# Kernel optimization log

Measured on AMD Instinct MI355X. Metric: run time of the kernel, lower is better.

Reference implementation:

```python
import jax, jax.numpy as jnp
import numpy as np

N = 100000        # num_nodes
F_IN = 512        # node_features
F_OUT = 2         # GCNConv out channels (hardcoded in module)
E = 3200000       # num edges (avg degree 32)


def setup_inputs() -> dict:
    key = jax.random.key(0)
    k = jax.random.split(key, 8)
    x = jax.random.normal(k[0], (N, F_IN), dtype=jnp.float32)
    edge_list = jax.random.randint(k[1], (2, E), 0, N, dtype=jnp.int64)
    edge_attr = jax.random.uniform(k[2], (E,), dtype=jnp.float32)
    # GCNConv params (glorot-ish scale)
    W = jax.random.normal(k[3], (F_IN, F_OUT), dtype=jnp.float32) / np.sqrt(F_IN)
    b = jnp.zeros((F_OUT,), dtype=jnp.float32)
    # fc head: Linear(num_nodes*2, 1)
    fc_w = jax.random.normal(k[4], (N * F_OUT,), dtype=jnp.float32) / np.sqrt(N * F_OUT)
    fc_b = jnp.zeros((), dtype=jnp.float32)
    return {"x": x, "edge_list": edge_list, "edge_attr": edge_attr,
            "W": W, "b": b, "fc_w": fc_w, "fc_b": fc_b}


def reference(x, edge_list, edge_attr, W, b, fc_w, fc_b):
    n = x.shape[0]
    row, col = edge_list[0], edge_list[1]
    # --- gcn_norm with add_self_loops=True (fill weight 1.0) ---
    loop = jnp.arange(n, dtype=edge_list.dtype)
    row_f = jnp.concatenate([row, loop])
    col_f = jnp.concatenate([col, loop])
    w_f = jnp.concatenate([edge_attr, jnp.ones((n,), dtype=edge_attr.dtype)])
    deg = jax.ops.segment_sum(w_f, col_f, num_segments=n)          # [N]
    deg_inv_sqrt = jnp.where(deg > 0, jax.lax.rsqrt(jnp.maximum(deg, 1e-30)), 0.0)
    norm = deg_inv_sqrt[row_f] * w_f * deg_inv_sqrt[col_f]          # [E+N]
    # --- linear transform then propagate (source row -> target col) ---
    h = x @ W                                                       # [N, 2]
    msg = h[row_f] * norm[:, None]                                  # [E+N, 2]
    out = jax.ops.segment_sum(msg, col_f, num_segments=n) + b      # [N, 2]
    # --- head: relu, (no dropout/noise: training=False), flatten, fc, sigmoid ---
    out = jax.nn.relu(out).reshape(-1)                              # [2N]
    logit = jnp.dot(out, fc_w) + fc_b
    return jax.nn.sigmoid(logit)
```

## Files before the change

kernel.cpp:

```cpp
#include <hip/hip_runtime.h>
#include <math.h>

#define N_NODES 100000
#define F_IN    512
#define E_EDGES 3200000

#define NR     16
#define RN     6250
#define SB     512
#define SCHUNK (E_EDGES / SB)
#define SLICES 32
#define JMASK  0x1FFF

__global__ __launch_bounds__(256) void k_hist(const int* __restrict__ col,
                                              int* __restrict__ cnt) {
    __shared__ int hcnt[NR];
    int t = threadIdx.x;
    if (t < NR) hcnt[t] = 0;
    __syncthreads();
    int base = blockIdx.x * SCHUNK;
    for (int i = t; i < SCHUNK; i += 256) {
        int r = col[base + i] / RN;
        atomicAdd(&hcnt[r], 1);
    }
    __syncthreads();
    if (t < NR) cnt[t * SB + blockIdx.x] = hcnt[t];
}

__global__ __launch_bounds__(1024) void k_prefix(const int* __restrict__ cnt,
                                                 int* __restrict__ off) {
    __shared__ int psum[1024];
    int t = threadIdx.x;
    int v[8]; int s = 0;
    int base = t * 8;
#pragma unroll
    for (int k = 0; k < 8; ++k) { v[k] = s; s += cnt[base + k]; }
    psum[t] = s;
    __syncthreads();
    for (int d = 1; d < 1024; d <<= 1) {
        int add = (t >= d) ? psum[t - d] : 0;
        __syncthreads();
        psum[t] += add;
        __syncthreads();
    }
    int excl = psum[t] - s;
#pragma unroll
    for (int k = 0; k < 8; ++k) off[base + k] = excl + v[k];
    if (t == 1023) off[NR * SB] = psum[1023];
}

__global__ __launch_bounds__(256) void k_scatter(const int* __restrict__ row,
                                                 const int* __restrict__ col,
                                                 const float* __restrict__ w,
                                                 const int* __restrict__ off,
                                                 unsigned* __restrict__ sidx,
                                                 float* __restrict__ sw) {
    __shared__ int cur[NR];
    int t = threadIdx.x;
    if (t < NR) cur[t] = off[t * SB + blockIdx.x];
    __syncthreads();
    int base = blockIdx.x * SCHUNK;
    for (int i = t; i < SCHUNK; i += 256) {
        int c  = col[base + i];
        int rr = row[base + i];
        float wv = w[base + i];
        int r = c / RN;
        int j = c - r * RN;
        int slot = atomicAdd(&cur[r], 1);
        sidx[slot] = (unsigned)j | ((unsigned)rr << 13);
        sw[slot]   = wv;
    }
}

__global__ __launch_bounds__(1024) void k_deg_s(const unsigned* __restrict__ sidx,
                                                const float* __restrict__ sw,
                                                const int* __restrict__ off,
                                                float* __restrict__ rep_deg) {
    __shared__ float sdeg[RN];
    int r = blockIdx.x / SLICES, s = blockIdx.x % SLICES;
    int lo_r = off[r * SB], hi_r = off[(r + 1) * SB];
    int len = hi_r - lo_r;
    int lo = lo_r + len * s / SLICES;
    int hi = lo_r + len * (s + 1) / SLICES;
    for (int j = threadIdx.x; j < RN; j += 1024) sdeg[j] = 0.0f;
    __syncthreads();
    for (int i = lo + threadIdx.x; i < hi; i += 1024) {
        unsigned u = sidx[i];
        atomicAdd(&sdeg[u & JMASK], sw[i]);
    }
    __syncthreads();
    float* out = rep_deg + (size_t)blockIdx.x * RN;
    for (int j = threadIdx.x; j < RN; j += 1024) out[j] = sdeg[j];
}

__global__ void k_dis(const float* __restrict__ rep_deg,
                      float* __restrict__ dis, float* __restrict__ logit) {
    int i = blockIdx.x * blockDim.x + threadIdx.x;
    if (i < N_NODES) {
        int r = i / RN, j = i - r * RN;
        const float* base = rep_deg + (size_t)(r * SLICES) * RN + j;
        float d = 1.0f;
#pragma unroll
        for (int p = 0; p < SLICES; ++p) d += base[p * RN];
        dis[i] = rsqrtf(d);
    }
    if (i == 0) logit[0] = 0.0f;
}

__global__ __launch_bounds__(256) void k_gemv(const float* __restrict__ x,
                                              const float* __restrict__ W,
                                              const float* __restrict__ dis,
                                              float* __restrict__ g) {
    int row  = (blockIdx.x * blockDim.x + threadIdx.x) >> 6;
    int lane = threadIdx.x & 63;
    if (row >= N_NODES) return;
    const float* xr = x + (size_t)row * F_IN;
    float a0 = 0.0f, a1 = 0.0f;
#pragma unroll
    for (int c = 0; c < 2; ++c) {
        int k = c * 256 + lane * 4;
        float4 xv  = *(const float4*)(xr + k);
        float4 w01 = *(const float4*)(W + 2 * k);
        float4 w23 = *(const float4*)(W + 2 * k + 4);
        a0 += xv.x * w01.x + xv.y * w01.z + xv.z * w23.x + xv.w * w23.z;
        a1 += xv.x * w01.y + xv.y * w01.w + xv.z * w23.y + xv.w * w23.w;
    }
#pragma unroll
    for (int off = 32; off > 0; off >>= 1) {
        a0 += __shfl_down(a0, off, 64);
        a1 += __shfl_down(a1, off, 64);
    }
    if (lane == 0) {
        float d = dis[row];
        g[2 * row]     = a0 * d;
        g[2 * row + 1] = a1 * d;
    }
}

__global__ __launch_bounds__(1024) void k_prop_s(const unsigned* __restrict__ sidx,
                                                 const float* __restrict__ sw,
                                                 const int* __restrict__ off,
                                                 const float* __restrict__ g,
                                                 float* __restrict__ rep_acc) {
    __shared__ float sacc[RN * 2];
    int r = blockIdx.x / SLICES, s = blockIdx.x % SLICES;
    int lo_r = off[r * SB], hi_r = off[(r + 1) * SB];
    int len = hi_r - lo_r;
    int lo = lo_r + len * s / SLICES;
    int hi = lo_r + len * (s + 1) / SLICES;
    for (int j = threadIdx.x; j < RN * 2; j += 1024) sacc[j] = 0.0f;
    __syncthreads();
    for (int i = lo + threadIdx.x; i < hi; i += 1024) {
        unsigned u = sidx[i];
        int j  = u & JMASK;
        int rr = u >> 13;
        float we = sw[i];
        float2 gv = *(const float2*)(g + 2 * rr);
        atomicAdd(&sacc[2 * j],     gv.x * we);
        atomicAdd(&sacc[2 * j + 1], gv.y * we);
    }
    __syncthreads();
    float* out = rep_acc + (size_t)blockIdx.x * (RN * 2);
    for (int j = threadIdx.x; j < RN * 2; j += 1024) out[j] = sacc[j];
}

__global__ __launch_bounds__(256) void k_epilogue(const float* __restrict__ rep_acc,
                                                  const float* __restrict__ g,
                                                  const float* __restrict__ dis,
                                                  const float* __restrict__ b,
                                                  const float* __restrict__ fc_w,
                                                  float* __restrict__ logit) {
    int i = blockIdx.x * blockDim.x + threadIdx.x;
    float partial = 0.0f;
    if (i < N_NODES) {
        int r = i / RN, j = i - r * RN;
        const float2* base = (const float2*)rep_acc + (size_t)(r * SLICES) * RN + j;
        float o0 = 0.0f, o1 = 0.0f;
#pragma unroll
        for (int p = 0; p < SLICES; ++p) { float2 v = base[p * RN]; o0 += v.x; o1 += v.y; }
        float d = dis[i];
        o0 = (o0 + g[2 * i])     * d + b[0];
        o1 = (o1 + g[2 * i + 1]) * d + b[1];
        o0 = fmaxf(o0, 0.0f); o1 = fmaxf(o1, 0.0f);
        partial = o0 * fc_w[2 * i] + o1 * fc_w[2 * i + 1];
    }
#pragma unroll
    for (int off = 32; off > 0; off >>= 1)
        partial += __shfl_down(partial, off, 64);
    __shared__ float sdata[4];
    int lane = threadIdx.x & 63, wid = threadIdx.x >> 6;
    if (lane == 0) sdata[wid] = partial;
    __syncthreads();
    if (threadIdx.x == 0)
        atomicAdd(logit, sdata[0] + sdata[1] + sdata[2] + sdata[3]);
}

__global__ void k_sigmoid(const float* __restrict__ logit,
                          const float* __restrict__ fc_b,
                          float* __restrict__ out) {
    float z = logit[0] + fc_b[0];
    out[0] = 1.0f / (1.0f + expf(-z));
}


__global__ void k_init_f(float* __restrict__ deg, float* __restrict__ accum,
                         float* __restrict__ logit) {
    int i = blockIdx.x * blockDim.x + threadIdx.x;
    if (i < N_NODES) {
        deg[i] = 1.0f;
        accum[2 * i] = 0.0f;
        accum[2 * i + 1] = 0.0f;
    }
    if (i == 0) logit[0] = 0.0f;
}

__global__ void k_deg_f(const int* __restrict__ col, const float* __restrict__ w,
                        float* __restrict__ deg) {
    int e = blockIdx.x * blockDim.x + threadIdx.x;
    if (e < E_EDGES) atomicAdd(&deg[col[e]], w[e]);
}

__global__ void k_rsqrt_f(float* __restrict__ deg) {
    int i = blockIdx.x * blockDim.x + threadIdx.x;
    if (i < N_NODES) deg[i] = rsqrtf(deg[i]);
}

__global__ void k_prop_f(const int* __restrict__ row, const int* __restrict__ col,
                         const float* __restrict__ w, const float* __restrict__ dis,
                         const float* __restrict__ g, float* __restrict__ accum) {
    int e = blockIdx.x * blockDim.x + threadIdx.x;
    if (e < E_EDGES) {
        int r = row[e], c = col[e];
        float nm = w[e];
        atomicAdd(&accum[2 * c],     g[2 * r] * nm);
        atomicAdd(&accum[2 * c + 1], g[2 * r + 1] * nm);
    }
}

__global__ __launch_bounds__(256) void k_epilogue_f(const float* __restrict__ accum,
                                                    const float* __restrict__ g,
                                                    const float* __restrict__ dis,
                                                    const float* __restrict__ b,
                                                    const float* __restrict__ fc_w,
                                                    float* __restrict__ logit) {
    int i = blockIdx.x * blockDim.x + threadIdx.x;
    float partial = 0.0f;
    if (i < N_NODES) {
        float d = dis[i];
        float o0 = (accum[2 * i]     + g[2 * i])     * d + b[0];
        float o1 = (accum[2 * i + 1] + g[2 * i + 1]) * d + b[1];
        o0 = fmaxf(o0, 0.0f); o1 = fmaxf(o1, 0.0f);
        partial = o0 * fc_w[2 * i] + o1 * fc_w[2 * i + 1];
    }
#pragma unroll
    for (int off = 32; off > 0; off >>= 1)
        partial += __shfl_down(partial, off, 64);
    __shared__ float sdata[4];
    int lane = threadIdx.x & 63, wid = threadIdx.x >> 6;
    if (lane == 0) sdata[wid] = partial;
    __syncthreads();
    if (threadIdx.x == 0)
        atomicAdd(logit, sdata[0] + sdata[1] + sdata[2] + sdata[3]);
}


extern "C" void kernel_launch(void* const* d_in, const int* in_sizes, int n_in,
                              void* d_out, int out_size, void* d_ws, size_t ws_size,
                              hipStream_t stream) {
    const float* x   = (const float*)d_in[0];
    const int*   el  = (const int*)d_in[1];
    const float* ea  = (const float*)d_in[2];
    const float* W   = (const float*)d_in[3];
    const float* b   = (const float*)d_in[4];
    const float* fcw = (const float*)d_in[5];
    const float* fcb = (const float*)d_in[6];
    float*       out = (float*)d_out;

    const int* row = el;
    const int* col = el + E_EDGES;

    float* ws = (float*)d_ws;
    const int TB = 256;
    dim3 gN((N_NODES + TB - 1) / TB);
    dim3 gG((N_NODES * 64 + TB - 1) / TB);

    size_t o_g    = 0;
    size_t o_dis  = o_g + 2 * N_NODES;
    size_t o_log  = o_dis + N_NODES;
    size_t o_cnt  = (o_log + 64) & ~63ull;
    size_t o_off  = o_cnt + NR * SB;
    size_t o_sidx = (o_off + NR * SB + 1 + 63) & ~63ull;
    size_t o_sw   = o_sidx + E_EDGES;
    size_t o_rd   = o_sw + E_EDGES;
    size_t o_ra   = o_rd + (size_t)NR * SLICES * RN;
    size_t need_fast = (o_ra + (size_t)NR * SLICES * RN * 2) * 4;

    if (ws_size >= need_fast) {
        float*    g       = ws + o_g;
        float*    dis     = ws + o_dis;
        float*    logit   = ws + o_log;
        int*      cnt     = (int*)(ws + o_cnt);
        int*      off     = (int*)(ws + o_off);
        unsigned* sidx    = (unsigned*)(ws + o_sidx);
        float*    sw      = ws + o_sw;
        float*    rep_deg = ws + o_rd;
        float*    rep_acc = ws + o_ra;

        k_hist    <<<SB, 256, 0, stream>>>(col, cnt);
        k_prefix  <<<1, 1024, 0, stream>>>(cnt, off);
        k_scatter <<<SB, 256, 0, stream>>>(row, col, ea, off, sidx, sw);
        k_deg_s   <<<NR * SLICES, 1024, 0, stream>>>(sidx, sw, off, rep_deg);
        k_dis     <<<gN, TB, 0, stream>>>(rep_deg, dis, logit);
        k_gemv    <<<gG, TB, 0, stream>>>(x, W, dis, g);
        k_prop_s  <<<NR * SLICES, 1024, 0, stream>>>(sidx, sw, off, g, rep_acc);
        k_epilogue<<<gN, TB, 0, stream>>>(rep_acc, g, dis, b, fcw, logit);
        k_sigmoid <<<1, 1, 0, stream>>>(logit, fcb, out);
    } else {
        float* deg   = ws;
        float* g     = ws + N_NODES;
        float* accum = ws + 3 * N_NODES;
        float* logit = ws + 5 * N_NODES;
        dim3 gE((E_EDGES + TB - 1) / TB);
        k_init_f    <<<gN, TB, 0, stream>>>(deg, accum, logit);
        k_deg_f     <<<gE, TB, 0, stream>>>(col, ea, deg);
        k_rsqrt_f   <<<gN, TB, 0, stream>>>(deg);
        k_gemv      <<<gG, TB, 0, stream>>>(x, W, deg, g);
        k_prop_f    <<<gE, TB, 0, stream>>>(row, col, ea, deg, g, accum);
        k_epilogue_f<<<gN, TB, 0, stream>>>(accum, g, deg, b, fcw, logit);
        k_sigmoid   <<<1, 1, 0, stream>>>(logit, fcb, out);
    }
}
```

Measured before the change: 411.2 us.

## Replace histogram-prefix-scatter with fixed-capacity buckets and global atomic cursors

```diff
diff --git a/kernel.cpp b/kernel.cpp
--- a/kernel.cpp
+++ b/kernel.cpp
@@ -9,12 +9,24 @@
 #define RN     6250
 #define SB     512
 #define SCHUNK (E_EDGES / SB)
+#define CAP    204800
 #define SLICES 32
 #define JMASK  0x1FFF
 
-__global__ __launch_bounds__(256) void k_hist(const int* __restrict__ col,
-                                              int* __restrict__ cnt) {
+__global__ void k_init(int* __restrict__ cursor, float* __restrict__ logit) {
+    int t = threadIdx.x;
+    if (t < NR) cursor[t] = t * CAP;
+    if (t == 0) logit[0] = 0.0f;
+}
+
+__global__ __launch_bounds__(256) void k_bucket(const int* __restrict__ row,
+                                                const int* __restrict__ col,
+                                                const float* __restrict__ w,
+                                                int* __restrict__ cursor,
+                                                unsigned* __restrict__ sidx,
+                                                float* __restrict__ sw) {
     __shared__ int hcnt[NR];
+    __shared__ int hbase[NR];
     int t = threadIdx.x;
     if (t < NR) hcnt[t] = 0;
     __syncthreads();
@@ -24,61 +36,29 @@
         atomicAdd(&hcnt[r], 1);
     }
     __syncthreads();
-    if (t < NR) cnt[t * SB + blockIdx.x] = hcnt[t];
-}
-
-__global__ __launch_bounds__(1024) void k_prefix(const int* __restrict__ cnt,
-                                                 int* __restrict__ off) {
-    __shared__ int psum[1024];
-    int t = threadIdx.x;
-    int v[8]; int s = 0;
-    int base = t * 8;
-#pragma unroll
-    for (int k = 0; k < 8; ++k) { v[k] = s; s += cnt[base + k]; }
-    psum[t] = s;
-    __syncthreads();
-    for (int d = 1; d < 1024; d <<= 1) {
-        int add = (t >= d) ? psum[t - d] : 0;
-        __syncthreads();
-        psum[t] += add;
-        __syncthreads();
-    }
-    int excl = psum[t] - s;
-#pragma unroll
-    for (int k = 0; k < 8; ++k) off[base + k] = excl + v[k];
-    if (t == 1023) off[NR * SB] = psum[1023];
-}
-
-__global__ __launch_bounds__(256) void k_scatter(const int* __restrict__ row,
-                                                 const int* __restrict__ col,
-                                                 const float* __restrict__ w,
-                                                 const int* __restrict__ off,
-                                                 unsigned* __restrict__ sidx,
-                                                 float* __restrict__ sw) {
-    __shared__ int cur[NR];
-    int t = threadIdx.x;
-    if (t < NR) cur[t] = off[t * SB + blockIdx.x];
-    __syncthreads();
-    int base = blockIdx.x * SCHUNK;
+    if (t < NR) {
+        hbase[t] = atomicAdd(&cursor[t], hcnt[t]);
+        hcnt[t] = 0;
+    }
+    __syncthreads();
     for (int i = t; i < SCHUNK; i += 256) {
-        int c  = col[base + i];
-        int rr = row[base + i];
-        float wv = w[base + i];
+        int c = col[base + i];
         int r = c / RN;
         int j = c - r * RN;
-        int slot = atomicAdd(&cur[r], 1);
-        sidx[slot] = (unsigned)j | ((unsigned)rr << 13);
-        sw[slot]   = wv;
+        int rank = atomicAdd(&hcnt[r], 1);
+        int slot = hbase[r] + rank;
+        sidx[slot] = (unsigned)j | ((unsigned)row[base + i] << 13);
+        sw[slot]   = w[base + i];
     }
 }
 
 __global__ __launch_bounds__(1024) void k_deg_s(const unsigned* __restrict__ sidx,
                                                 const float* __restrict__ sw,
-                                                const int* __restrict__ off,
+                                                const int* __restrict__ cursor,
                                                 float* __restrict__ rep_deg) {
     __shared__ float sdeg[RN];
     int r = blockIdx.x / SLICES, s = blockIdx.x % SLICES;
-    int lo_r = off[r * SB], hi_r = off[(r + 1) * SB];
+    int lo_r = r * CAP, hi_r = cursor[r];
     int len = hi_r - lo_r;
     int lo = lo_r + len * s / SLICES;
     int hi = lo_r + len * (s + 1) / SLICES;
@@ -94,7 +74,7 @@
 }
 
 __global__ void k_dis(const float* __restrict__ rep_deg,
-                      float* __restrict__ dis, float* __restrict__ logit) {
+                      float* __restrict__ dis) {
     int i = blockIdx.x * blockDim.x + threadIdx.x;
     if (i < N_NODES) {
         int r = i / RN, j = i - r * RN;
@@ -104,7 +84,6 @@
         for (int p = 0; p < SLICES; ++p) d += base[p * RN];
         dis[i] = rsqrtf(d);
     }
-    if (i == 0) logit[0] = 0.0f;
 }
 
 __global__ __launch_bounds__(256) void k_gemv(const float* __restrict__ x,
@@ -139,12 +118,12 @@
 
 __global__ __launch_bounds__(1024) void k_prop_s(const unsigned* __restrict__ sidx,
                                                  const float* __restrict__ sw,
-                                                 const int* __restrict__ off,
+                                                 const int* __restrict__ cursor,
                                                  const float* __restrict__ g,
                                                  float* __restrict__ rep_acc) {
     __shared__ float sacc[RN * 2];
     int r = blockIdx.x / SLICES, s = blockIdx.x % SLICES;
-    int lo_r = off[r * SB], hi_r = off[(r + 1) * SB];
+    int lo_r = r * CAP, hi_r = cursor[r];
     int len = hi_r - lo_r;
     int lo = lo_r + len * s / SLICES;
     int hi = lo_r + len * (s + 1) / SLICES;
@@ -287,11 +266,10 @@
     size_t o_g    = 0;
     size_t o_dis  = o_g + 2 * N_NODES;
     size_t o_log  = o_dis + N_NODES;
-    size_t o_cnt  = (o_log + 64) & ~63ull;
-    size_t o_off  = o_cnt + NR * SB;
-    size_t o_sidx = (o_off + NR * SB + 1 + 63) & ~63ull;
-    size_t o_sw   = o_sidx + E_EDGES;
-    size_t o_rd   = o_sw + E_EDGES;
+    size_t o_cur  = (o_log + 64) & ~63ull;
+    size_t o_sidx = (o_cur + 64) & ~63ull;
+    size_t o_sw   = o_sidx + (size_t)NR * CAP;
+    size_t o_rd   = o_sw + (size_t)NR * CAP;
     size_t o_ra   = o_rd + (size_t)NR * SLICES * RN;
     size_t need_fast = (o_ra + (size_t)NR * SLICES * RN * 2) * 4;
 
@@ -299,20 +277,18 @@
         float*    g       = ws + o_g;
         float*    dis     = ws + o_dis;
         float*    logit   = ws + o_log;
-        int*      cnt     = (int*)(ws + o_cnt);
-        int*      off     = (int*)(ws + o_off);
+        int*      cursor  = (int*)(ws + o_cur);
         unsigned* sidx    = (unsigned*)(ws + o_sidx);
         float*    sw      = ws + o_sw;
         float*    rep_deg = ws + o_rd;
         float*    rep_acc = ws + o_ra;
 
-        k_hist    <<<SB, 256, 0, stream>>>(col, cnt);
-        k_prefix  <<<1, 1024, 0, stream>>>(cnt, off);
-        k_scatter <<<SB, 256, 0, stream>>>(row, col, ea, off, sidx, sw);
-        k_deg_s   <<<NR * SLICES, 1024, 0, stream>>>(sidx, sw, off, rep_deg);
-        k_dis     <<<gN, TB, 0, stream>>>(rep_deg, dis, logit);
+        k_init    <<<1, 64, 0, stream>>>(cursor, logit);
+        k_bucket  <<<SB, 256, 0, stream>>>(row, col, ea, cursor, sidx, sw);
+        k_deg_s   <<<NR * SLICES, 1024, 0, stream>>>(sidx, sw, cursor, rep_deg);
+        k_dis     <<<gN, TB, 0, stream>>>(rep_deg, dis);
         k_gemv    <<<gG, TB, 0, stream>>>(x, W, dis, g);
-        k_prop_s  <<<NR * SLICES, 1024, 0, stream>>>(sidx, sw, off, g, rep_acc);
+        k_prop_s  <<<NR * SLICES, 1024, 0, stream>>>(sidx, sw, cursor, g, rep_acc);
         k_epilogue<<<gN, TB, 0, stream>>>(rep_acc, g, dis, b, fcw, logit);
         k_sigmoid <<<1, 1, 0, stream>>>(logit, fcb, out);
     } else {
```

New measurement: 415.1 us. About the same (+0.9%).
